# Kernel optimization log

Measured on AMD Instinct MI355X. Metric: run time of the kernel, lower is better.

## Reference

```python
import jax, jax.numpy as jnp
import numpy as np

EMBED_DIM = 1024
N_HEADS = 16
B, L = 2, 2048


def setup_inputs() -> dict:
    key = jax.random.key(0)
    ks = jax.random.split(key, 7)
    D = EMBED_DIM
    s = 1.0 / np.sqrt(D)
    return {
        "inputs": jax.random.normal(ks[0], (B, L, D), dtype=jnp.float32),
        "rotation_params": jax.random.normal(ks[1], (D, D), dtype=jnp.float32) * s,
        "entangle_params": jax.random.uniform(ks[2], (N_HEADS,), dtype=jnp.float32, minval=0.5, maxval=1.5),
        "Wq": jax.random.normal(ks[3], (D, D), dtype=jnp.float32) * s,
        "Wk": jax.random.normal(ks[4], (D, D), dtype=jnp.float32) * s,
        "Wv": jax.random.normal(ks[5], (D, D), dtype=jnp.float32) * s,
        "Wo": jax.random.normal(ks[6], (D, D), dtype=jnp.float32) * s,
    }


def reference(inputs, rotation_params, entangle_params, Wq, Wk, Wv, Wo):
    Bq, Lq, D = inputs.shape
    H = N_HEADS
    hd = D // H
    # Linear (no bias, torch convention x @ W.T) followed by rotation matmul
    Q = (inputs @ Wq.T) @ rotation_params
    K = (inputs @ Wk.T) @ rotation_params
    V = (inputs @ Wv.T) @ rotation_params
    # split heads: (B, H, L, hd)
    Q = Q.reshape(Bq, Lq, H, hd).transpose(0, 2, 1, 3)
    K = K.reshape(Bq, Lq, H, hd).transpose(0, 2, 1, 3)
    V = V.reshape(Bq, Lq, H, hd).transpose(0, 2, 1, 3)
    scale = entangle_params.reshape(1, H, 1, 1) / jnp.sqrt(jnp.asarray(hd, dtype=inputs.dtype))
    scores = jnp.einsum("bhqd,bhkd->bhqk", Q, K) * scale
    attn = jax.nn.softmax(scores, axis=-1)  # dropout inert (eval / p=0)
    out = jnp.einsum("bhqk,bhkd->bhqd", attn, V)
    out = out.transpose(0, 2, 1, 3).reshape(Bq, Lq, D)
    return out @ Wo.T
```

## Files before the change

kernel.cpp:

```cpp
#include <hip/hip_runtime.h>
#include <cstdint>
#include <cstddef>

typedef __attribute__((ext_vector_type(8))) short  bf16x8;
typedef __attribute__((ext_vector_type(8))) _Float16 f16x8;
typedef __attribute__((ext_vector_type(4))) _Float16 f16x4;
typedef __attribute__((ext_vector_type(4))) float  f32x4;
typedef __attribute__((ext_vector_type(4))) unsigned short u16x4;
typedef __attribute__((ext_vector_type(2))) unsigned int u32x2;

#define LOG2E 1.44269504088896340736f
#define PBIAS 6.0f

__device__ __forceinline__ unsigned short f2bf(float f) {
  unsigned int u = __builtin_bit_cast(unsigned int, f);
  u += 0x7fffu + ((u >> 16) & 1u);
  return (unsigned short)(u >> 16);
}
__device__ __forceinline__ float bf2f(unsigned short s) {
  unsigned int u = ((unsigned int)s) << 16;
  return __builtin_bit_cast(float, u);
}

__device__ __forceinline__ float fast_exp2(float x) {
  return __builtin_amdgcn_exp2f(x);
}

__device__ __forceinline__ void gll16(const void* g, void* l) {
  __builtin_amdgcn_global_load_lds(
      (const __attribute__((address_space(1))) unsigned int*)g,
      (__attribute__((address_space(3))) unsigned int*)l, 16, 0, 0);
}

__global__ __launch_bounds__(256) void prep(
    const float* __restrict__ x,  unsigned short* __restrict__ xb,
    const float* __restrict__ Wo, unsigned short* __restrict__ Wob,
    const float* __restrict__ R,  const float* __restrict__ Wq,
    const float* __restrict__ Wk, const float* __restrict__ Wv,
    unsigned short* __restrict__ RT,  unsigned short* __restrict__ WqT,
    unsigned short* __restrict__ WkT, unsigned short* __restrict__ WvT) {
  int bid = blockIdx.x;
  __shared__ unsigned short s[64][68];
  if (bid < 5120) {
    const float* src = bid < 4096 ? x : Wo;
    unsigned short* dst = bid < 4096 ? xb : Wob;
    int i = (bid < 4096 ? bid : bid - 4096) * 256 + threadIdx.x;
    float4 v = ((const float4*)src)[i];
    u16x4 o;
    o[0] = f2bf(v.x); o[1] = f2bf(v.y); o[2] = f2bf(v.z); o[3] = f2bf(v.w);
    ((u16x4*)dst)[i] = o;
    return;
  }
  int t = bid - 5120;
  int z = t >> 8, tile = t & 255;
  const float* in = z == 0 ? R : (z == 1 ? Wq : (z == 2 ? Wk : Wv));
  unsigned short* out = z == 0 ? RT : (z == 1 ? WqT : (z == 2 ? WkT : WvT));
  int r0 = (tile >> 4) * 64, c0 = (tile & 15) * 64;
  int tt = threadIdx.x;
  int tr = tt >> 4, tc4 = (tt & 15) * 4;
  for (int i = 0; i < 4; ++i) {
    int r = tr + i * 16;
    float4 v = *(const float4*)(in + (size_t)(r0 + r) * 1024 + c0 + tc4);
    s[r][tc4 + 0] = f2bf(v.x); s[r][tc4 + 1] = f2bf(v.y);
    s[r][tc4 + 2] = f2bf(v.z); s[r][tc4 + 3] = f2bf(v.w);
  }
  __syncthreads();
  for (int i = 0; i < 4; ++i) {
    int oc = tr + i * 16;
    u16x4 o;
    o[0] = s[tc4 + 0][oc]; o[1] = s[tc4 + 1][oc];
    o[2] = s[tc4 + 2][oc]; o[3] = s[tc4 + 3][oc];
    *(u16x4*)(out + (size_t)(c0 + oc) * 1024 + r0 + tc4) = o;
  }
}

__global__ void tr_v(const unsigned short* __restrict__ in, unsigned short* __restrict__ out) {
  __shared__ unsigned short s[64][68];
  int t = threadIdx.x;
  int r0 = blockIdx.y * 64, c0 = blockIdx.x * 64;
  int tr = t >> 4, tc4 = (t & 15) * 4;
  for (int i = 0; i < 4; ++i) {
    int r = tr + i * 16;
    u16x4 v = *(const u16x4*)(in + (size_t)(r0 + r) * 1024 + c0 + tc4);
    s[r][tc4 + 0] = v[0]; s[r][tc4 + 1] = v[1]; s[r][tc4 + 2] = v[2]; s[r][tc4 + 3] = v[3];
  }
  __syncthreads();
  for (int i = 0; i < 4; ++i) {
    int oc = tr + i * 16;
    u16x4 o;
#pragma unroll
    for (int j = 0; j < 4; ++j) {
      _Float16 h = (_Float16)bf2f(s[tc4 + j][oc]);
      o[j] = __builtin_bit_cast(unsigned short, h);
    }
    int col = r0 + tc4;
    int c32 = col & 31;
    int pos = (col & ~31) + ((c32 >> 2) & 3) * 8 + (c32 >> 4) * 4;
    *(u16x4*)(out + (size_t)(c0 + oc) * 4096 + pos) = o;
  }
}

template <bool BF16OUT>
__global__ __launch_bounds__(256) void gemm_nt(
    const unsigned short* __restrict__ A,
    const unsigned short* __restrict__ B0, const unsigned short* __restrict__ B1,
    const unsigned short* __restrict__ B2,
    void* __restrict__ C0, void* __restrict__ C1, void* __restrict__ C2,
    int M, int N, int K) {
  const unsigned short* B = blockIdx.z == 0 ? B0 : (blockIdx.z == 1 ? B1 : B2);
  void* Cv = blockIdx.z == 0 ? C0 : (blockIdx.z == 1 ? C1 : C2);

  __shared__ unsigned short As[128 * 64];
  __shared__ unsigned short Bs[128 * 64];

  int tid = threadIdx.x, w = tid >> 6, lane = tid & 63;
  int lo = lane & 15, quad = lane >> 4;
  int m0 = blockIdx.y * 128, n0 = blockIdx.x * 128;
  int wm = (w >> 1) * 64, wn = (w & 1) * 64;

  f32x4 z4 = {0.f, 0.f, 0.f, 0.f};
  f32x4 acc[4][4];
  for (int mi = 0; mi < 4; ++mi)
    for (int ni = 0; ni < 4; ++ni) acc[mi][ni] = z4;

  int rloc = lane >> 3;
  int srcChunk = (lane & 7) ^ (rloc & 7);
  int cbase = w * 4;
  const unsigned short* Ag = A + (size_t)(m0 + cbase * 8 + rloc) * K + srcChunk * 8;
  const unsigned short* Bg = B + (size_t)(n0 + cbase * 8 + rloc) * K + srcChunk * 8;
  int ldsOfs = cbase * 512 + lane * 8;
  int cx0 = (quad ^ (lane & 7)) * 8;
  int cx1 = ((quad + 4) ^ (lane & 7)) * 8;

  for (int k0 = 0; k0 < K; k0 += 64) {
#pragma unroll
    for (int j = 0; j < 4; ++j) {
      gll16(Ag + (size_t)j * 8 * K + k0, As + ldsOfs + j * 512);
      gll16(Bg + (size_t)j * 8 * K + k0, Bs + ldsOfs + j * 512);
    }
    __syncthreads();
#pragma unroll
    for (int ks = 0; ks < 2; ++ks) {
      int cx = ks ? cx1 : cx0;
      bf16x8 af[4], bfr[4];
#pragma unroll
      for (int mi = 0; mi < 4; ++mi)
        af[mi] = *(const bf16x8*)(As + (wm + mi * 16 + lo) * 64 + cx);
#pragma unroll
      for (int ni = 0; ni < 4; ++ni)
        bfr[ni] = *(const bf16x8*)(Bs + (wn + ni * 16 + lo) * 64 + cx);
#pragma unroll
      for (int mi = 0; mi < 4; ++mi)
#pragma unroll
        for (int ni = 0; ni < 4; ++ni)
          acc[mi][ni] = __builtin_amdgcn_mfma_f32_16x16x32_bf16(af[mi], bfr[ni], acc[mi][ni], 0, 0, 0);
    }
    __syncthreads();
  }

#pragma unroll
  for (int mi = 0; mi < 4; ++mi)
#pragma unroll
    for (int ni = 0; ni < 4; ++ni)
      for (int i = 0; i < 4; ++i) {
        int r = m0 + wm + mi * 16 + quad * 4 + i;
        int c = n0 + wn + ni * 16 + lo;
        if (BF16OUT)
          ((unsigned short*)Cv)[(size_t)r * N + c] = f2bf(acc[mi][ni][i]);
        else
          ((float*)Cv)[(size_t)r * N + c] = acc[mi][ni][i];
      }
}

__global__ __launch_bounds__(256, 2) void flash_attn(
    const unsigned short* __restrict__ Q, const unsigned short* __restrict__ Kg_,
    const unsigned short* __restrict__ Vt, const float* __restrict__ ent,
    unsigned short* __restrict__ O) {
  int tid = threadIdx.x, w = tid >> 6, lane = tid & 63;
  int lo = lane & 15, quad = lane >> 4;

  int bid = blockIdx.x;
  int g = (bid & 7) + 8 * (bid >> 7);
  int qt = (bid >> 3) & 15;
  int b = g >> 4, h = g & 15;
  int q0 = qt * 128;
  float scale = ent[h] * (0.125f * LOG2E);

  __shared__ unsigned short Ks[2][64 * 64];
  __shared__ unsigned short Vts[2][64 * 64];

  bf16x8 aq[2][2];
#pragma unroll
  for (int f = 0; f < 2; ++f)
#pragma unroll
    for (int ks = 0; ks < 2; ++ks) {
      uint4 v = *(const uint4*)(Q + (size_t)(b * 2048 + q0 + w * 32 + f * 16 + lo) * 1024 +
                                h * 64 + ks * 32 + quad * 8);
      unsigned int* pv = (unsigned int*)&v;
      uint4 o; unsigned int* po = (unsigned int*)&o;
#pragma unroll
      for (int j = 0; j < 4; ++j) {
        float f0 = bf2f((unsigned short)(pv[j] & 0xffffu)) * scale;
        float f1 = bf2f((unsigned short)(pv[j] >> 16)) * scale;
        po[j] = (unsigned int)f2bf(f0) | ((unsigned int)f2bf(f1) << 16);
      }
      aq[f][ks] = *(bf16x8*)&o;
    }

  f32x4 binit = {-PBIAS, -PBIAS, -PBIAS, -PBIAS};
  f32x4 z4 = {0.f, 0.f, 0.f, 0.f};
  f32x4 acco[4][2];
#pragma unroll
  for (int di = 0; di < 4; ++di) {
    acco[di][0] = z4; acco[di][1] = z4;
  }
  float lsum0 = 0.f, lsum1 = 0.f;

  int rloc = lane >> 3;
  int srcChunk = (lane & 7) ^ (rloc & 7);
  int cb = w * 2;
  const unsigned short* Kp = Kg_ + (size_t)(b * 2048) * 1024 + h * 64;
  const unsigned short* Vp = Vt + (size_t)(h * 64) * 4096 + (size_t)b * 2048;
  int cx0 = (quad ^ (lane & 7)) * 8;
  int cx1 = ((quad + 4) ^ (lane & 7)) * 8;

#pragma unroll
  for (int j = 0; j < 2; ++j) {
    int c = cb + j;
    int r = c * 8 + rloc;
    gll16(Kp + (size_t)r * 1024 + srcChunk * 8, Ks[0] + c * 512 + lane * 8);
    gll16(Vp + (size_t)r * 4096 + srcChunk * 8, Vts[0] + c * 512 + lane * 8);
  }

  for (int it = 0; it < 32; ++it) {
    int buf = it & 1;
    __syncthreads();
    if (it + 1 < 32) {
      int kvn = (it + 1) * 64;
#pragma unroll
      for (int j = 0; j < 2; ++j) {
        int c = cb + j;
        int r = c * 8 + rloc;
        gll16(Kp + (size_t)(kvn + r) * 1024 + srcChunk * 8, Ks[buf ^ 1] + c * 512 + lane * 8);
        gll16(Vp + (size_t)r * 4096 + kvn + srcChunk * 8, Vts[buf ^ 1] + c * 512 + lane * 8);
      }
    }
    const unsigned short* Kb_ = Ks[buf];
    const unsigned short* Vb_ = Vts[buf];

    f32x4 accs[4][2];
    __builtin_amdgcn_s_setprio(1);
#pragma unroll
    for (int kt = 0; kt < 4; ++kt) {
      bf16x8 kf0 = *(const bf16x8*)(Kb_ + (kt * 16 + lo) * 64 + cx0);
      bf16x8 kf1 = *(const bf16x8*)(Kb_ + (kt * 16 + lo) * 64 + cx1);
#pragma unroll
      for (int f = 0; f < 2; ++f) {
        f32x4 a = __builtin_amdgcn_mfma_f32_16x16x32_bf16(kf0, aq[f][0], binit, 0, 0, 0);
        accs[kt][f] = __builtin_amdgcn_mfma_f32_16x16x32_bf16(kf1, aq[f][1], a, 0, 0, 0);
      }
    }
    __builtin_amdgcn_s_setprio(0);

    f16x4 ap[4][2];
#pragma unroll
    for (int kt = 0; kt < 4; ++kt) {
#pragma unroll
      for (int f = 0; f < 2; ++f) {
        float p0 = fast_exp2(accs[kt][f][0]);
        float p1 = fast_exp2(accs[kt][f][1]);
        float p2 = fast_exp2(accs[kt][f][2]);
        float p3 = fast_exp2(accs[kt][f][3]);
        if (f == 0) lsum0 += (p0 + p1) + (p2 + p3);
        else        lsum1 += (p0 + p1) + (p2 + p3);
        u32x2 uu;
        uu[0] = __builtin_bit_cast(unsigned int, __builtin_amdgcn_cvt_pkrtz(p0, p1));
        uu[1] = __builtin_bit_cast(unsigned int, __builtin_amdgcn_cvt_pkrtz(p2, p3));
        ap[kt][f] = __builtin_bit_cast(f16x4, uu);
      }
    }

    __builtin_amdgcn_s_setprio(1);
#pragma unroll
    for (int t2 = 0; t2 < 2; ++t2) {
      f16x8 a80 = __builtin_shufflevector(ap[2 * t2][0], ap[2 * t2 + 1][0], 0, 1, 2, 3, 4, 5, 6, 7);
      f16x8 a81 = __builtin_shufflevector(ap[2 * t2][1], ap[2 * t2 + 1][1], 0, 1, 2, 3, 4, 5, 6, 7);
#pragma unroll
      for (int di = 0; di < 4; ++di) {
        f16x8 bv8 = *(const f16x8*)(Vb_ + (di * 16 + lo) * 64 +
                                    (((t2 * 4 + quad) ^ (lo & 7)) << 3));
        acco[di][0] = __builtin_amdgcn_mfma_f32_16x16x32_f16(a80, bv8, acco[di][0], 0, 0, 0);
        acco[di][1] = __builtin_amdgcn_mfma_f32_16x16x32_f16(a81, bv8, acco[di][1], 0, 0, 0);
      }
    }
    __builtin_amdgcn_s_setprio(0);
  }

#pragma unroll
  for (int f = 0; f < 2; ++f) {
    float v = f == 0 ? lsum0 : lsum1;
    v += __shfl_xor(v, 16);
    v += __shfl_xor(v, 32);
    float inv = 1.0f / v;

#pragma unroll
    for (int i = 0; i < 4; ++i) {
      float invq = __shfl(inv, quad * 4 + i);
#pragma unroll
      for (int di = 0; di < 4; ++di) {
        size_t ofs = (size_t)(b * 2048 + q0 + w * 32 + f * 16 + quad * 4 + i) * 1024 +
                     h * 64 + di * 16 + lo;
        O[ofs] = f2bf(acco[di][f][i] * invq);
      }
    }
  }
}

extern "C" void kernel_launch(void* const* d_in, const int* in_sizes, int n_in,
                              void* d_out, int out_size, void* d_ws, size_t ws_size,
                              hipStream_t stream) {
  const float* x   = (const float*)d_in[0];
  const float* R   = (const float*)d_in[1];
  const float* ent = (const float*)d_in[2];
  const float* Wq  = (const float*)d_in[3];
  const float* Wk  = (const float*)d_in[4];
  const float* Wv  = (const float*)d_in[5];
  const float* Wo  = (const float*)d_in[6];
  float* out = (float*)d_out;

  const size_t MLD = (size_t)4096 * 1024;
  const size_t DD  = (size_t)1024 * 1024;
  if (ws_size < (MLD * 6 + DD * 8) * 2) return;

  unsigned short* ws  = (unsigned short*)d_ws;
  unsigned short* xb  = ws;
  unsigned short* RT  = xb + MLD;
  unsigned short* WqT = RT + DD;
  unsigned short* WkT = WqT + DD;
  unsigned short* WvT = WkT + DD;
  unsigned short* Wob = WvT + DD;
  unsigned short* AqT = Wob + DD;
  unsigned short* AkT = AqT + DD;
  unsigned short* AvT = AkT + DD;
  unsigned short* Qb  = AvT + DD;
  unsigned short* Kb  = Qb + MLD;
  unsigned short* Vb  = Kb + MLD;
  unsigned short* Vtf = Vb + MLD;
  unsigned short* aO  = Vtf + MLD;

  prep<<<dim3(6144), dim3(256), 0, stream>>>(
      x, xb, Wo, Wob, R, Wq, Wk, Wv, RT, WqT, WkT, WvT);

  gemm_nt<true><<<dim3(8, 8, 3), dim3(256), 0, stream>>>(
      RT, WqT, WkT, WvT, (void*)AqT, (void*)AkT, (void*)AvT, 1024, 1024, 1024);
  gemm_nt<true><<<dim3(8, 32, 3), dim3(256), 0, stream>>>(
      xb, AqT, AkT, AvT, (void*)Qb, (void*)Kb, (void*)Vb, 4096, 1024, 1024);
  tr_v<<<dim3(16, 64), dim3(256), 0, stream>>>(Vb, Vtf);
  flash_attn<<<dim3(512), dim3(256), 0, stream>>>(Qb, Kb, Vtf, ent, aO);
  gemm_nt<false><<<dim3(8, 32, 1), dim3(256), 0, stream>>>(
      aO, Wob, Wob, Wob, (void*)out, (void*)out, (void*)out, 4096, 1024, 1024);
}
```

Measured before the change: 210.5 us.

## Split KV range across two warp groups in flash attention and reduce via LDS

Doubles the flash attention block to 512 threads, with each half of the warps processing half of the key/value sequence into its own double-buffered LDS region. After the loop, the second half writes its partial output accumulators and row sums to LDS, and the first half adds them and normalizes. This raises the warp count per CU for the fixed 512-block grid to improve latency hiding. In exchange it adds an LDS reduction, an extra barrier, and higher register pressure from the new launch bounds.

```diff
diff --git a/kernel.cpp b/kernel.cpp
--- a/kernel.cpp
+++ b/kernel.cpp
@@ -172,12 +172,13 @@
       }
 }
 
-__global__ __launch_bounds__(256, 2) void flash_attn(
+__global__ __launch_bounds__(512, 4) void flash_attn(
     const unsigned short* __restrict__ Q, const unsigned short* __restrict__ Kg_,
     const unsigned short* __restrict__ Vt, const float* __restrict__ ent,
     unsigned short* __restrict__ O) {
   int tid = threadIdx.x, w = tid >> 6, lane = tid & 63;
   int lo = lane & 15, quad = lane >> 4;
+  int half = w >> 2, wl = w & 3;
 
   int bid = blockIdx.x;
   int g = (bid & 7) + 8 * (bid >> 7);
@@ -186,15 +187,14 @@
   int q0 = qt * 128;
   float scale = ent[h] * (0.125f * LOG2E);
 
-  __shared__ unsigned short Ks[2][64 * 64];
-  __shared__ unsigned short Vts[2][64 * 64];
+  __shared__ unsigned short lds[32768];
 
   bf16x8 aq[2][2];
 #pragma unroll
   for (int f = 0; f < 2; ++f)
 #pragma unroll
     for (int ks = 0; ks < 2; ++ks) {
-      uint4 v = *(const uint4*)(Q + (size_t)(b * 2048 + q0 + w * 32 + f * 16 + lo) * 1024 +
+      uint4 v = *(const uint4*)(Q + (size_t)(b * 2048 + q0 + wl * 32 + f * 16 + lo) * 1024 +
                                 h * 64 + ks * 32 + quad * 8);
       unsigned int* pv = (unsigned int*)&v;
       uint4 o; unsigned int* po = (unsigned int*)&o;
@@ -218,35 +218,38 @@
 
   int rloc = lane >> 3;
   int srcChunk = (lane & 7) ^ (rloc & 7);
-  int cb = w * 2;
-  const unsigned short* Kp = Kg_ + (size_t)(b * 2048) * 1024 + h * 64;
-  const unsigned short* Vp = Vt + (size_t)(h * 64) * 4096 + (size_t)b * 2048;
+  int cb = wl * 2;
+  const unsigned short* Kp = Kg_ + (size_t)(b * 2048 + half * 1024) * 1024 + h * 64;
+  const unsigned short* Vp = Vt + (size_t)(h * 64) * 4096 + (size_t)(b * 2048 + half * 1024);
   int cx0 = (quad ^ (lane & 7)) * 8;
   int cx1 = ((quad + 4) ^ (lane & 7)) * 8;
+
+  unsigned short* Kh = lds + half * 2 * 4096;
+  unsigned short* Vh = lds + 16384 + half * 2 * 4096;
 
 #pragma unroll
   for (int j = 0; j < 2; ++j) {
     int c = cb + j;
     int r = c * 8 + rloc;
-    gll16(Kp + (size_t)r * 1024 + srcChunk * 8, Ks[0] + c * 512 + lane * 8);
-    gll16(Vp + (size_t)r * 4096 + srcChunk * 8, Vts[0] + c * 512 + lane * 8);
-  }
-
-  for (int it = 0; it < 32; ++it) {
+    gll16(Kp + (size_t)r * 1024 + srcChunk * 8, Kh + c * 512 + lane * 8);
+    gll16(Vp + (size_t)r * 4096 + srcChunk * 8, Vh + c * 512 + lane * 8);
+  }
+
+  for (int it = 0; it < 16; ++it) {
     int buf = it & 1;
     __syncthreads();
-    if (it + 1 < 32) {
+    if (it + 1 < 16) {
       int kvn = (it + 1) * 64;
 #pragma unroll
       for (int j = 0; j < 2; ++j) {
         int c = cb + j;
         int r = c * 8 + rloc;
-        gll16(Kp + (size_t)(kvn + r) * 1024 + srcChunk * 8, Ks[buf ^ 1] + c * 512 + lane * 8);
-        gll16(Vp + (size_t)r * 4096 + kvn + srcChunk * 8, Vts[buf ^ 1] + c * 512 + lane * 8);
-      }
-    }
-    const unsigned short* Kb_ = Ks[buf];
-    const unsigned short* Vb_ = Vts[buf];
+        gll16(Kp + (size_t)(kvn + r) * 1024 + srcChunk * 8, Kh + (buf ^ 1) * 4096 + c * 512 + lane * 8);
+        gll16(Vp + (size_t)r * 4096 + kvn + srcChunk * 8, Vh + (buf ^ 1) * 4096 + c * 512 + lane * 8);
+      }
+    }
+    const unsigned short* Kb_ = Kh + buf * 4096;
+    const unsigned short* Vb_ = Vh + buf * 4096;
 
     f32x4 accs[4][2];
     __builtin_amdgcn_s_setprio(1);
@@ -296,6 +299,33 @@
     __builtin_amdgcn_s_setprio(0);
   }
 
+  __syncthreads();
+  float* cm = (float*)lds;
+  float* base = cm + wl * 2304;
+  if (half == 1) {
+#pragma unroll
+    for (int di = 0; di < 4; ++di)
+#pragma unroll
+      for (int f = 0; f < 2; ++f)
+#pragma unroll
+        for (int i = 0; i < 4; ++i)
+          base[(di * 8 + f * 4 + i) * 64 + lane] = acco[di][f][i];
+    base[32 * 64 + lane] = lsum0;
+    base[33 * 64 + lane] = lsum1;
+  }
+  __syncthreads();
+  if (half == 1) return;
+
+#pragma unroll
+  for (int di = 0; di < 4; ++di)
+#pragma unroll
+    for (int f = 0; f < 2; ++f)
+#pragma unroll
+      for (int i = 0; i < 4; ++i)
+        acco[di][f][i] += base[(di * 8 + f * 4 + i) * 64 + lane];
+  lsum0 += base[32 * 64 + lane];
+  lsum1 += base[33 * 64 + lane];
+
 #pragma unroll
   for (int f = 0; f < 2; ++f) {
     float v = f == 0 ? lsum0 : lsum1;
@@ -308,7 +338,7 @@
       float invq = __shfl(inv, quad * 4 + i);
 #pragma unroll
       for (int di = 0; di < 4; ++di) {
-        size_t ofs = (size_t)(b * 2048 + q0 + w * 32 + f * 16 + quad * 4 + i) * 1024 +
+        size_t ofs = (size_t)(b * 2048 + q0 + wl * 32 + f * 16 + quad * 4 + i) * 1024 +
                      h * 64 + di * 16 + lo;
         O[ofs] = f2bf(acco[di][f][i] * invq);
       }
@@ -356,7 +386,7 @@
   gemm_nt<true><<<dim3(8, 32, 3), dim3(256), 0, stream>>>(
       xb, AqT, AkT, AvT, (void*)Qb, (void*)Kb, (void*)Vb, 4096, 1024, 1024);
   tr_v<<<dim3(16, 64), dim3(256), 0, stream>>>(Vb, Vtf);
-  flash_attn<<<dim3(512), dim3(256), 0, stream>>>(Qb, Kb, Vtf, ent, aO);
+  flash_attn<<<dim3(512), dim3(512), 0, stream>>>(Qb, Kb, Vtf, ent, aO);
   gemm_nt<false><<<dim3(8, 32, 1), dim3(256), 0, stream>>>(
       aO, Wob, Wob, Wob, (void*)out, (void*)out, (void*)out, 4096, 1024, 1024);
 }
```

Result: faster. 204.7 us (-2.8%).
